# Optimization experiments

Hardware: AMD Instinct MI355X
Metric: run time of the kernel (lower is better)

Reference implementation:

```python
import math
import jax, jax.numpy as jnp
import numpy as np

DIM = 2048
N_HEADS = 16
HEAD_DIM = DIM // N_HEADS  # 128
BSZ = 2
SEQLEN = 2048
ROPE_THETA = 500000.0


def _make_freqs(seqlen, head_dim, theta):
    inv = 1.0 / (theta ** (np.arange(0, head_dim, 2, dtype=np.float32) / head_dim))
    t = np.arange(seqlen, dtype=np.float32)
    f = np.outer(t, inv)  # [S, hd//2]
    return jnp.asarray(np.cos(f)), jnp.asarray(np.sin(f))


def setup_inputs() -> dict:
    key = jax.random.key(0)
    kx, kq, kk, kv, ko = jax.random.split(key, 5)
    scale = 0.02
    x = jax.random.normal(kx, (BSZ, SEQLEN, DIM), dtype=jnp.float32)
    wq = jax.random.normal(kq, (DIM, DIM), dtype=jnp.float32) * scale
    wk = jax.random.normal(kk, (DIM, DIM), dtype=jnp.float32) * scale
    wv = jax.random.normal(kv, (DIM, DIM), dtype=jnp.float32) * scale
    wo = jax.random.normal(ko, (DIM, DIM), dtype=jnp.float32) * scale
    freqs_cos, freqs_sin = _make_freqs(SEQLEN, HEAD_DIM, ROPE_THETA)
    # causal additive mask: 0 on/below diag, -inf above
    mask = jnp.triu(jnp.full((SEQLEN, SEQLEN), float('-inf'), dtype=jnp.float32), k=1)
    return {"x": x, "start_pos": 0, "freqs_cos": freqs_cos, "freqs_sin": freqs_sin,
            "mask": mask, "wq": wq, "wk": wk, "wv": wv, "wo": wo}


def _apply_rope(t, cos, sin):
    # t: [B, S, H, hd]; cos/sin: [S, hd//2]
    b, s, h, hd = t.shape
    tr = t.reshape(b, s, h, hd // 2, 2)
    a, bb = tr[..., 0], tr[..., 1]
    c = cos[None, :, None, :]
    sn = sin[None, :, None, :]
    out_r = a * c - bb * sn
    out_i = a * sn + bb * c
    return jnp.stack([out_r, out_i], axis=-1).reshape(b, s, h, hd)


def reference(x, start_pos, freqs_cos, freqs_sin, mask, wq, wk, wv, wo):
    b, s, _ = x.shape
    xq = (x @ wq.T).reshape(b, s, N_HEADS, HEAD_DIM)
    xk = (x @ wk.T).reshape(b, s, N_HEADS, HEAD_DIM)
    xv = (x @ wv.T).reshape(b, s, N_HEADS, HEAD_DIM)
    xq = _apply_rope(xq, freqs_cos, freqs_sin)
    xk = _apply_rope(xk, freqs_cos, freqs_sin)
    # [B, H, S, hd]
    xq = xq.transpose(0, 2, 1, 3)
    xk = xk.transpose(0, 2, 1, 3)
    xv = xv.transpose(0, 2, 1, 3)
    scores = jnp.einsum('bhqd,bhkd->bhqk', xq, xk) / math.sqrt(HEAD_DIM)
    scores = scores + mask[None, None, :, :]
    probs = jax.nn.softmax(scores.astype(jnp.float32), axis=-1).astype(xq.dtype)
    out = jnp.einsum('bhqk,bhkd->bhqd', probs, xv)
    out = out.transpose(0, 2, 1, 3).reshape(b, s, -1)
    return out @ wo.T
```

## Files before the change

### kernel.cpp

```cpp
#include <hip/hip_runtime.h>
#include <stdint.h>

#define DIM 2048
#define SEQ 2048
#define NHEADS 16
#define HDIM 128
#define BSZ 2
#define ROWS (BSZ*SEQ)

typedef uint16_t u16;
typedef __attribute__((ext_vector_type(8))) short bf16x8;
typedef __attribute__((ext_vector_type(4))) short bf16x4;
typedef __attribute__((ext_vector_type(4))) float fx4;
typedef __attribute__((ext_vector_type(4))) uint16_t u16x4;

typedef const __attribute__((address_space(1))) uint32_t* gp_t;
typedef __attribute__((address_space(3))) uint32_t* lp_t;
#define GLL16(g, l) __builtin_amdgcn_global_load_lds((gp_t)(g), (lp_t)(l), 16, 0, 0)

__device__ inline u16 f2bf(float f) {
  union { float f; uint32_t u; } v; v.f = f;
  uint32_t u = v.u;
  u += 0x7FFFu + ((u >> 16) & 1u);
  return (u16)(u >> 16);
}
__device__ inline float bf2f(u16 h) {
  union { uint32_t u; float f; } v; v.u = ((uint32_t)h) << 16;
  return v.f;
}

__global__ __launch_bounds__(256) void cvt5_kernel(const float* __restrict__ sx,
    const float* __restrict__ s1, const float* __restrict__ s2,
    const float* __restrict__ s3, const float* __restrict__ s4,
    u16* __restrict__ dst) {
  const int XC = (ROWS * DIM) / 4;
  const int WC = (DIM * DIM) / 4;
  int i = blockIdx.x * 256 + threadIdx.x;
  const float* src;
  int off;
  if (i < XC) { src = sx; off = i; }
  else {
    int t = i - XC;
    int w = t >> 20;
    off = t & (WC - 1);
    src = (w == 0) ? s1 : (w == 1) ? s2 : (w == 2) ? s3 : s4;
  }
  fx4 f = *(const fx4*)(src + (size_t)off * 4);
  u16x4 o;
  o[0] = f2bf(f[0]); o[1] = f2bf(f[1]); o[2] = f2bf(f[2]); o[3] = f2bf(f[3]);
  *(u16x4*)(dst + (size_t)i * 4) = o;
}

__device__ inline void gemm128_core(const u16* __restrict__ A, const u16* __restrict__ B,
                                    u16 (&As)[128][32], u16 (&Bs)[128][32],
                                    fx4 (&acc)[4][4], int M0, int N0) {
  const int tid  = threadIdx.x;
  const int lane = tid & 63;
  const int wave = tid >> 6;
  const int wm = (wave >> 1) * 64;
  const int wn = (wave & 1) * 64;
  const int l16 = lane & 15;
  const int q8  = (lane >> 4) * 8;
#pragma unroll
  for (int tm = 0; tm < 4; ++tm)
#pragma unroll
    for (int tn = 0; tn < 4; ++tn) acc[tm][tn] = fx4{0.f, 0.f, 0.f, 0.f};

  const int wrow = wave * 32;
  const size_t laneA = (size_t)(M0 + wrow + (lane >> 2)) * DIM + (lane & 3) * 8;
  const size_t laneB = (size_t)(N0 + wrow + (lane >> 2)) * DIM + (lane & 3) * 8;

  for (int k0 = 0; k0 < DIM; k0 += 32) {
    __syncthreads();
    GLL16(A + laneA + k0,            &As[wrow][0]);
    GLL16(A + laneA + 16 * DIM + k0, &As[wrow + 16][0]);
    GLL16(B + laneB + k0,            &Bs[wrow][0]);
    GLL16(B + laneB + 16 * DIM + k0, &Bs[wrow + 16][0]);
    __syncthreads();
    bf16x8 af[4], bfr[4];
#pragma unroll
    for (int t = 0; t < 4; ++t) {
      af[t]  = *(const bf16x8*)&As[wm + t * 16 + l16][q8];
      bfr[t] = *(const bf16x8*)&Bs[wn + t * 16 + l16][q8];
    }
#pragma unroll
    for (int tm = 0; tm < 4; ++tm)
#pragma unroll
      for (int tn = 0; tn < 4; ++tn)
        acc[tm][tn] = __builtin_amdgcn_mfma_f32_16x16x32_bf16(af[tm], bfr[tn], acc[tm][tn], 0, 0, 0);
  }
}

#define BM 256
#define BN 128
#define BK 64
#define NT (DIM / BK)
#define BUFSZ ((BM + BN) * BK)

__global__ __launch_bounds__(512, 2) void gemm_qkv8(const u16* __restrict__ A,
    const u16* __restrict__ B0, const u16* __restrict__ B1, const u16* __restrict__ B2,
    u16* __restrict__ C0, u16* __restrict__ C1, u16* __restrict__ vtg,
    const float* __restrict__ fcos, const float* __restrict__ fsin) {
  __shared__ __align__(16) u16 sm[2 * BUFSZ];

  const int tid  = threadIdx.x;
  const int lane = tid & 63, wave = tid >> 6;
  const int l16  = lane & 15, quad = lane >> 4;
  const int wm   = wave >> 2;
  const int wn   = wave & 3;

  int t = (blockIdx.x & 7) * 96 + (blockIdx.x >> 3);
  const int z   = t >> 8;
  const int rem = t & 255;
  const int M0  = (rem >> 4) * BM;
  const int N0  = (rem & 15) * BN;
  const u16* B = (z == 0) ? B0 : (z == 1) ? B1 : B2;

  const int u0 = tid, u1 = 512 + tid;
  const int rl0 = u0 >> 3, ch0 = (u0 & 7) ^ (rl0 & 7);
  const int rl1 = u1 >> 3, ch1 = (u1 & 7) ^ (rl1 & 7);

  const int sw  = l16 & 7;
  const int ka0 = (quad ^ sw) * 8;
  const int ka1 = ((4 + quad) ^ sw) * 8;
  const int rowA = (wm * 128 + l16) * BK;
  const int rowB = (wn * 32  + l16) * BK;

#define STGA(h, kt2) do { if ((kt2) < NT) {                                              \
    const u16* _g = A + (size_t)(M0 + (h) * 128) * DIM + (kt2) * BK;                     \
    u16* _l = sm + ((kt2) & 1) * BUFSZ + (h) * 8192 + wave * 512;                        \
    GLL16(_g + (size_t)rl0 * DIM + ch0 * 8, _l);                                         \
    GLL16(_g + (size_t)rl1 * DIM + ch1 * 8, _l + 4096); } } while (0)
#define STGB(kt2) do { if ((kt2) < NT) {                                                 \
    const u16* _g = B + (size_t)N0 * DIM + (kt2) * BK;                                   \
    u16* _l = sm + ((kt2) & 1) * BUFSZ + 16384 + wave * 512;                             \
    GLL16(_g + (size_t)rl0 * DIM + ch0 * 8, _l);                                         \
    GLL16(_g + (size_t)rl1 * DIM + ch1 * 8, _l + 4096); } } while (0)

  STGB(0); STGA(0, 0); STGA(1, 0);
  STGB(1); STGA(0, 1);
  asm volatile("s_waitcnt vmcnt(4)" ::: "memory");
  __builtin_amdgcn_s_barrier();

  fx4 acc[8][2];
#pragma unroll
  for (int m = 0; m < 8; ++m)
#pragma unroll
    for (int n = 0; n < 2; ++n) acc[m][n] = fx4{0.f, 0.f, 0.f, 0.f};

  bf16x8 af[4][2], b0[2], b1[2];

  for (int kt = 0; kt < NT; ++kt) {
    const u16* Ab = sm + (kt & 1) * BUFSZ;
    const u16* Bb = Ab + 16384;

#pragma unroll
    for (int m = 0; m < 4; ++m) {
      af[m][0] = *(const bf16x8*)(Ab + rowA + m * (16 * BK) + ka0);
      af[m][1] = *(const bf16x8*)(Ab + rowA + m * (16 * BK) + ka1);
    }
    b0[0] = *(const bf16x8*)(Bb + rowB + ka0);
    b0[1] = *(const bf16x8*)(Bb + rowB + ka1);
    STGA(1, kt + 1);
    asm volatile("s_waitcnt lgkmcnt(8)" ::: "memory");
    __builtin_amdgcn_sched_barrier(0);
    __builtin_amdgcn_s_barrier();
    asm volatile("s_waitcnt lgkmcnt(0)" ::: "memory");
    __builtin_amdgcn_sched_barrier(0);
    __builtin_amdgcn_s_setprio(1);
#pragma unroll
    for (int m = 0; m < 4; ++m) {
      acc[m][0] = __builtin_amdgcn_mfma_f32_16x16x32_bf16(af[m][0], b0[0], acc[m][0], 0, 0, 0);
      acc[m][0] = __builtin_amdgcn_mfma_f32_16x16x32_bf16(af[m][1], b0[1], acc[m][0], 0, 0, 0);
    }
    __builtin_amdgcn_s_setprio(0);
    __builtin_amdgcn_s_barrier();

    b1[0] = *(const bf16x8*)(Bb + rowB + 16 * BK + ka0);
    b1[1] = *(const bf16x8*)(Bb + rowB + 16 * BK + ka1);
    __builtin_amdgcn_s_barrier();
    asm volatile("s_waitcnt lgkmcnt(0)" ::: "memory");
    __builtin_amdgcn_sched_barrier(0);
    __builtin_amdgcn_s_setprio(1);
#pragma unroll
    for (int m = 0; m < 4; ++m) {
      acc[m][1] = __builtin_amdgcn_mfma_f32_16x16x32_bf16(af[m][0], b1[0], acc[m][1], 0, 0, 0);
      acc[m][1] = __builtin_amdgcn_mfma_f32_16x16x32_bf16(af[m][1], b1[1], acc[m][1], 0, 0, 0);
    }
    __builtin_amdgcn_s_setprio(0);
    __builtin_amdgcn_s_barrier();

#pragma unroll
    for (int m = 0; m < 4; ++m) {
      af[m][0] = *(const bf16x8*)(Ab + rowA + (m + 4) * (16 * BK) + ka0);
      af[m][1] = *(const bf16x8*)(Ab + rowA + (m + 4) * (16 * BK) + ka1);
    }
    STGB(kt + 2);
    __builtin_amdgcn_s_barrier();
    asm volatile("s_waitcnt lgkmcnt(0)" ::: "memory");
    __builtin_amdgcn_sched_barrier(0);
    __builtin_amdgcn_s_setprio(1);
#pragma unroll
    for (int m = 0; m < 4; ++m) {
      acc[m + 4][1] = __builtin_amdgcn_mfma_f32_16x16x32_bf16(af[m][0], b1[0], acc[m + 4][1], 0, 0, 0);
      acc[m + 4][1] = __builtin_amdgcn_mfma_f32_16x16x32_bf16(af[m][1], b1[1], acc[m + 4][1], 0, 0, 0);
    }
    __builtin_amdgcn_s_setprio(0);
    __builtin_amdgcn_s_barrier();

    STGA(0, kt + 2);
    __builtin_amdgcn_s_barrier();
    __builtin_amdgcn_s_setprio(1);
#pragma unroll
    for (int m = 0; m < 4; ++m) {
      acc[m + 4][0] = __builtin_amdgcn_mfma_f32_16x16x32_bf16(af[m][0], b0[0], acc[m + 4][0], 0, 0, 0);
      acc[m + 4][0] = __builtin_amdgcn_mfma_f32_16x16x32_bf16(af[m][1], b0[1], acc[m + 4][0], 0, 0, 0);
    }
    __builtin_amdgcn_s_setprio(0);
    if (kt < NT - 2) asm volatile("s_waitcnt vmcnt(4)" ::: "memory");
    else             asm volatile("s_waitcnt vmcnt(0)" ::: "memory");
    __builtin_amdgcn_sched_barrier(0);
    __builtin_amdgcn_s_barrier();
  }
#undef STGA
#undef STGB

  if (z < 2) {
    u16* C = (z == 0) ? C0 : C1;
    u16* Cr = C + (size_t)(M0 + wm * 128 + quad * 4) * DIM + N0 + wn * 32 + l16;
#pragma unroll
    for (int mt = 0; mt < 8; ++mt)
#pragma unroll
      for (int r = 0; r < 4; ++r) {
        int s = (M0 + wm * 128 + mt * 16 + quad * 4 + r) & (SEQ - 1);
        const float* cb = fcos + s * 64;
        const float* sb = fsin + s * 64;
#pragma unroll
        for (int nt = 0; nt < 2; ++nt) {
          int p = (wn * 32 + nt * 16 + l16) >> 1;
          float val = acc[mt][nt][r];
          float par = __shfl_xor(val, 1);
          float c = cb[p], sn = sb[p];
          float out = (l16 & 1) ? (par * sn + val * c) : (val * c - par * sn);
          Cr[(size_t)(mt * 16 + r) * DIM + nt * 16] = f2bf(out);
        }
      }
  } else {
    u16 (*T)[256] = reinterpret_cast<u16 (*)[256]>(sm);
    __syncthreads();
#pragma unroll
    for (int mt = 0; mt < 8; ++mt)
#pragma unroll
      for (int nt = 0; nt < 2; ++nt) {
        int col = wn * 32 + nt * 16 + l16;
        int rowb = (wm * 128 + mt * 16 + quad * 4) ^ ((col & 7) << 3);
        u16x4 p;
        p[0] = f2bf(acc[mt][nt][0]); p[1] = f2bf(acc[mt][nt][1]);
        p[2] = f2bf(acc[mt][nt][2]); p[3] = f2bf(acc[mt][nt][3]);
        *(u16x4*)&T[col][rowb] = p;
      }
    __syncthreads();
    const int b  = M0 >> 11;
    const int s0 = M0 & (SEQ - 1);
    const int h  = N0 >> 7;
#pragma unroll
    for (int i = 0; i < 8; ++i) {
      int c = i * 512 + tid;
      int col = c >> 5;
      int s8 = (c & 31) * 8;
      bf16x8 v8 = *(const bf16x8*)&T[col][s8 ^ ((col & 7) << 3)];
      *(bf16x8*)(vtg + ((size_t)(b * NHEADS + h) * HDIM + col) * SEQ + s0 + s8) = v8;
    }
  }
}

__global__ __launch_bounds__(256) void gemm_out(const u16* __restrict__ A,
                                                const u16* __restrict__ B,
                                                float* __restrict__ C) {
  __shared__ __align__(16) u16 As[128][32];
  __shared__ __align__(16) u16 Bs[128][32];
  const int M0 = blockIdx.y * 128, N0 = blockIdx.x * 128;
  fx4 acc[4][4];
  gemm128_core(A, B, As, Bs, acc, M0, N0);
  const int lane = threadIdx.x & 63, wave = threadIdx.x >> 6;
  const int wm = (wave >> 1) * 64, wn = (wave & 1) * 64;
  const int l16 = lane & 15, quad = lane >> 4;
#pragma unroll
  for (int tm = 0; tm < 4; ++tm)
#pragma unroll
    for (int tn = 0; tn < 4; ++tn)
#pragma unroll
      for (int r = 0; r < 4; ++r) {
        size_t row = (size_t)(M0 + wm + tm * 16 + quad * 4 + r);
        size_t col = (size_t)(N0 + wn + tn * 16 + l16);
        C[row * DIM + col] = acc[tm][tn][r];
      }
}

struct SMemS { u16 Ks[64][136]; u16 Vt[128][72]; };
union SMemU { SMemS s; u16 Ot[4][32][136]; };

__global__ __launch_bounds__(256, 2) void attn_kernel(const u16* __restrict__ qm,
                                                      const u16* __restrict__ km,
                                                      const u16* __restrict__ vtg,
                                                      u16* __restrict__ ao) {
  __shared__ __align__(16) SMemU sm;
  const int tid = threadIdx.x;
  const int lane = tid & 63, wave = tid >> 6;
  const int l16 = lane & 15, quad = lane >> 4;
  const int idx = blockIdx.x;
  const int bh = idx & 31;
  const int j = idx >> 5;
  const int qt = (j < 8) ? (15 - j) : (j - 8);
  const int b = bh >> 4, h = bh & 15;
  const int q0 = qt * 128;
  const size_t brow = (size_t)b * SEQ;
  const int hc = h * HDIM;
  const size_t vbase = (size_t)bh * HDIM * SEQ;
  const int nkt = 2 * qt + 2;

  bf16x8 aq[2][4];
#pragma unroll
  for (int nt = 0; nt < 2; ++nt) {
    size_t qbase = (brow + q0 + wave * 32 + nt * 16 + l16) * DIM + hc;
#pragma unroll
    for (int dc = 0; dc < 4; ++dc)
      aq[nt][dc] = *(const bf16x8*)(qm + qbase + dc * 32 + quad * 8);
  }
  fx4 o[2][8];
#pragma unroll
  for (int nt = 0; nt < 2; ++nt)
#pragma unroll
    for (int dt = 0; dt < 8; ++dt) o[nt][dt] = fx4{0.f, 0.f, 0.f, 0.f};
  float mr[2] = {-3e38f, -3e38f}, lr[2] = {0.f, 0.f};

  bf16x8 kreg[4], vreg[4];
#pragma unroll
  for (int i = 0; i < 4; ++i) {
    int c = i * 256 + tid;
    kreg[i] = *(const bf16x8*)(km + (brow + (c >> 4)) * DIM + hc + (c & 15) * 8);
    vreg[i] = *(const bf16x8*)(vtg + vbase + (size_t)(c >> 3) * SEQ + (c & 7) * 8);
  }

  for (int kt = 0; kt < nkt; ++kt) {
    __syncthreads();
#pragma unroll
    for (int i = 0; i < 4; ++i) {
      int c = i * 256 + tid;
      *(bf16x8*)&sm.s.Ks[c >> 4][(c & 15) * 8] = kreg[i];
      *(bf16x8*)&sm.s.Vt[c >> 3][(c & 7) * 8] = vreg[i];
    }
    __syncthreads();
    if (kt + 1 < nkt) {
      const int kv1 = (kt + 1) * 64;
#pragma unroll
      for (int i = 0; i < 4; ++i) {
        int c = i * 256 + tid;
        kreg[i] = *(const bf16x8*)(km + (brow + kv1 + (c >> 4)) * DIM + hc + (c & 15) * 8);
        vreg[i] = *(const bf16x8*)(vtg + vbase + (size_t)(c >> 3) * SEQ + kv1 + (c & 7) * 8);
      }
    }
    fx4 s[2][4];
#pragma unroll
    for (int tm = 0; tm < 4; ++tm) {
      fx4 a0 = fx4{0.f, 0.f, 0.f, 0.f}, a1 = fx4{0.f, 0.f, 0.f, 0.f};
#pragma unroll
      for (int dc = 0; dc < 4; ++dc) {
        bf16x8 kf = *(const bf16x8*)&sm.s.Ks[tm * 16 + l16][dc * 32 + quad * 8];
        a0 = __builtin_amdgcn_mfma_f32_16x16x32_bf16(kf, aq[0][dc], a0, 0, 0, 0);
        a1 = __builtin_amdgcn_mfma_f32_16x16x32_bf16(kf, aq[1][dc], a1, 0, 0, 0);
      }
      s[0][tm] = a0 * 0.08838834764831845f;
      s[1][tm] = a1 * 0.08838834764831845f;
    }
    if (kt >= nkt - 2) {
      const int kv0 = kt * 64;
#pragma unroll
      for (int nt = 0; nt < 2; ++nt) {
        int qpos = q0 + wave * 32 + nt * 16 + l16;
#pragma unroll
        for (int tm = 0; tm < 4; ++tm)
#pragma unroll
          for (int r = 0; r < 4; ++r)
            if (kv0 + tm * 16 + quad * 4 + r > qpos) s[nt][tm][r] = -1e30f;
      }
    }
    float alpha[2];
    bf16x4 pf[2][4];
#pragma unroll
    for (int nt = 0; nt < 2; ++nt) {
      float t = -3e38f;
#pragma unroll
      for (int tm = 0; tm < 4; ++tm)
        t = fmaxf(t, fmaxf(fmaxf(s[nt][tm][0], s[nt][tm][1]),
                           fmaxf(s[nt][tm][2], s[nt][tm][3])));
      t = fmaxf(t, __shfl_xor(t, 16));
      t = fmaxf(t, __shfl_xor(t, 32));
      float mnew = fmaxf(mr[nt], t);
      alpha[nt] = __expf(mr[nt] - mnew);
      float sum = 0.f;
#pragma unroll
      for (int tm = 0; tm < 4; ++tm) {
        fx4 p;
#pragma unroll
        for (int r = 0; r < 4; ++r) {
          p[r] = __expf(s[nt][tm][r] - mnew);
          sum += p[r];
        }
        bf16x4 pb;
        pb[0] = (short)f2bf(p[0]); pb[1] = (short)f2bf(p[1]);
        pb[2] = (short)f2bf(p[2]); pb[3] = (short)f2bf(p[3]);
        pf[nt][tm] = pb;
      }
      sum += __shfl_xor(sum, 16);
      sum += __shfl_xor(sum, 32);
      lr[nt] = lr[nt] * alpha[nt] + sum;
      mr[nt] = mnew;
#pragma unroll
      for (int dt = 0; dt < 8; ++dt) o[nt][dt] *= alpha[nt];
    }
#pragma unroll
    for (int tm = 0; tm < 4; ++tm) {
#pragma unroll
      for (int dt = 0; dt < 8; ++dt) {
        bf16x4 vf = *(const bf16x4*)&sm.s.Vt[dt * 16 + l16][tm * 16 + quad * 4];
        o[0][dt] = __builtin_amdgcn_mfma_f32_16x16x16bf16_1k(vf, pf[0][tm], o[0][dt], 0, 0, 0);
        o[1][dt] = __builtin_amdgcn_mfma_f32_16x16x16bf16_1k(vf, pf[1][tm], o[1][dt], 0, 0, 0);
      }
    }
  }
  __syncthreads();
#pragma unroll
  for (int nt = 0; nt < 2; ++nt) {
    float inv = 1.f / lr[nt];
#pragma unroll
    for (int dt = 0; dt < 8; ++dt) {
      fx4 v = o[nt][dt];
      u16x4 p;
      p[0] = f2bf(v[0] * inv); p[1] = f2bf(v[1] * inv);
      p[2] = f2bf(v[2] * inv); p[3] = f2bf(v[3] * inv);
      *(u16x4*)&sm.Ot[wave][nt * 16 + l16][dt * 16 + quad * 4] = p;
    }
  }
#pragma unroll
  for (int i = 0; i < 8; ++i) {
    int c = i * 64 + lane;
    int row = c >> 4;
    int ch = c & 15;
    bf16x8 t = *(const bf16x8*)&sm.Ot[wave][row][ch * 8];
    *(bf16x8*)(ao + (brow + q0 + wave * 32 + row) * DIM + hc + ch * 8) = t;
  }
}

extern "C" void kernel_launch(void* const* d_in, const int* in_sizes, int n_in,
                              void* d_out, int out_size, void* d_ws, size_t ws_size,
                              hipStream_t stream) {
  const float* x    = (const float*)d_in[0];
  const float* fcos = (const float*)d_in[2];
  const float* fsin = (const float*)d_in[3];
  const float* wq   = (const float*)d_in[5];
  const float* wk   = (const float*)d_in[6];
  const float* wv   = (const float*)d_in[7];
  const float* wo   = (const float*)d_in[8];
  float* out = (float*)d_out;

  const size_t XN = (size_t)ROWS * DIM;
  const size_t WN = (size_t)DIM * DIM;
  u16* ws  = (u16*)d_ws;
  u16* xb  = ws;
  u16* wqb = xb + XN;
  u16* wkb = wqb + WN;
  u16* wvb = wkb + WN;
  u16* wob = wvb + WN;
  u16* q   = wob + WN;
  u16* k   = q + XN;
  u16* vtg = k + XN;
  u16* ao  = vtg + XN;

  const int total_chunks = (int)((XN + 4 * WN) / 4);
  cvt5_kernel<<<total_chunks / 256, 256, 0, stream>>>(x, wq, wk, wv, wo, ws);

  gemm_qkv8<<<dim3(768), 512, 0, stream>>>(xb, wqb, wkb, wvb, q, k, vtg, fcos, fsin);

  attn_kernel<<<dim3(512), 256, 0, stream>>>(q, k, vtg, ao);

  gemm_out<<<dim3(DIM / 128, ROWS / 128), 256, 0, stream>>>(ao, wob, out);
}
```

Baseline: 387.4 us.

## Replace output projection GEMM with 8-wave double-buffered 256x128 pipelined kernel

New measurement: 388.4 us. About the same (+0.2%).

```diff
diff --git a/kernel.cpp b/kernel.cpp
--- a/kernel.cpp
+++ b/kernel.cpp
@@ -51,46 +51,6 @@
   *(u16x4*)(dst + (size_t)i * 4) = o;
 }
 
-__device__ inline void gemm128_core(const u16* __restrict__ A, const u16* __restrict__ B,
-                                    u16 (&As)[128][32], u16 (&Bs)[128][32],
-                                    fx4 (&acc)[4][4], int M0, int N0) {
-  const int tid  = threadIdx.x;
-  const int lane = tid & 63;
-  const int wave = tid >> 6;
-  const int wm = (wave >> 1) * 64;
-  const int wn = (wave & 1) * 64;
-  const int l16 = lane & 15;
-  const int q8  = (lane >> 4) * 8;
-#pragma unroll
-  for (int tm = 0; tm < 4; ++tm)
-#pragma unroll
-    for (int tn = 0; tn < 4; ++tn) acc[tm][tn] = fx4{0.f, 0.f, 0.f, 0.f};
-
-  const int wrow = wave * 32;
-  const size_t laneA = (size_t)(M0 + wrow + (lane >> 2)) * DIM + (lane & 3) * 8;
-  const size_t laneB = (size_t)(N0 + wrow + (lane >> 2)) * DIM + (lane & 3) * 8;
-
-  for (int k0 = 0; k0 < DIM; k0 += 32) {
-    __syncthreads();
-    GLL16(A + laneA + k0,            &As[wrow][0]);
-    GLL16(A + laneA + 16 * DIM + k0, &As[wrow + 16][0]);
-    GLL16(B + laneB + k0,            &Bs[wrow][0]);
-    GLL16(B + laneB + 16 * DIM + k0, &Bs[wrow + 16][0]);
-    __syncthreads();
-    bf16x8 af[4], bfr[4];
-#pragma unroll
-    for (int t = 0; t < 4; ++t) {
-      af[t]  = *(const bf16x8*)&As[wm + t * 16 + l16][q8];
-      bfr[t] = *(const bf16x8*)&Bs[wn + t * 16 + l16][q8];
-    }
-#pragma unroll
-    for (int tm = 0; tm < 4; ++tm)
-#pragma unroll
-      for (int tn = 0; tn < 4; ++tn)
-        acc[tm][tn] = __builtin_amdgcn_mfma_f32_16x16x32_bf16(af[tm], bfr[tn], acc[tm][tn], 0, 0, 0);
-  }
-}
-
 #define BM 256
 #define BN 128
 #define BK 64
@@ -274,27 +234,138 @@
   }
 }
 
-__global__ __launch_bounds__(256) void gemm_out(const u16* __restrict__ A,
-                                                const u16* __restrict__ B,
-                                                float* __restrict__ C) {
-  __shared__ __align__(16) u16 As[128][32];
-  __shared__ __align__(16) u16 Bs[128][32];
-  const int M0 = blockIdx.y * 128, N0 = blockIdx.x * 128;
-  fx4 acc[4][4];
-  gemm128_core(A, B, As, Bs, acc, M0, N0);
-  const int lane = threadIdx.x & 63, wave = threadIdx.x >> 6;
-  const int wm = (wave >> 1) * 64, wn = (wave & 1) * 64;
-  const int l16 = lane & 15, quad = lane >> 4;
-#pragma unroll
-  for (int tm = 0; tm < 4; ++tm)
-#pragma unroll
-    for (int tn = 0; tn < 4; ++tn)
-#pragma unroll
-      for (int r = 0; r < 4; ++r) {
-        size_t row = (size_t)(M0 + wm + tm * 16 + quad * 4 + r);
-        size_t col = (size_t)(N0 + wn + tn * 16 + l16);
-        C[row * DIM + col] = acc[tm][tn][r];
-      }
+__global__ __launch_bounds__(512, 2) void gemm_out8(const u16* __restrict__ A,
+                                                    const u16* __restrict__ B,
+                                                    float* __restrict__ C) {
+  __shared__ __align__(16) u16 sm[2 * BUFSZ];
+
+  const int tid  = threadIdx.x;
+  const int lane = tid & 63, wave = tid >> 6;
+  const int l16  = lane & 15, quad = lane >> 4;
+  const int wm   = wave >> 2;
+  const int wn   = wave & 3;
+
+  int t = (blockIdx.x & 7) * 32 + (blockIdx.x >> 3);
+  const int M0  = (t >> 4) * BM;
+  const int N0  = (t & 15) * BN;
+
+  const int u0 = tid, u1 = 512 + tid;
+  const int rl0 = u0 >> 3, ch0 = (u0 & 7) ^ (rl0 & 7);
+  const int rl1 = u1 >> 3, ch1 = (u1 & 7) ^ (rl1 & 7);
+
+  const int sw  = l16 & 7;
+  const int ka0 = (quad ^ sw) * 8;
+  const int ka1 = ((4 + quad) ^ sw) * 8;
+  const int rowA = (wm * 128 + l16) * BK;
+  const int rowB = (wn * 32  + l16) * BK;
+
+#define STGA(h, kt2) do { if ((kt2) < NT) {                                              \
+    const u16* _g = A + (size_t)(M0 + (h) * 128) * DIM + (kt2) * BK;                     \
+    u16* _l = sm + ((kt2) & 1) * BUFSZ + (h) * 8192 + wave * 512;                        \
+    GLL16(_g + (size_t)rl0 * DIM + ch0 * 8, _l);                                         \
+    GLL16(_g + (size_t)rl1 * DIM + ch1 * 8, _l + 4096); } } while (0)
+#define STGB(kt2) do { if ((kt2) < NT) {                                                 \
+    const u16* _g = B + (size_t)N0 * DIM + (kt2) * BK;                                   \
+    u16* _l = sm + ((kt2) & 1) * BUFSZ + 16384 + wave * 512;                             \
+    GLL16(_g + (size_t)rl0 * DIM + ch0 * 8, _l);                                         \
+    GLL16(_g + (size_t)rl1 * DIM + ch1 * 8, _l + 4096); } } while (0)
+
+  STGB(0); STGA(0, 0); STGA(1, 0);
+  STGB(1); STGA(0, 1);
+  asm volatile("s_waitcnt vmcnt(4)" ::: "memory");
+  __builtin_amdgcn_s_barrier();
+
+  fx4 acc[8][2];
+#pragma unroll
+  for (int m = 0; m < 8; ++m)
+#pragma unroll
+    for (int n = 0; n < 2; ++n) acc[m][n] = fx4{0.f, 0.f, 0.f, 0.f};
+
+  bf16x8 af[4][2], b0[2], b1[2];
+
+  for (int kt = 0; kt < NT; ++kt) {
+    const u16* Ab = sm + (kt & 1) * BUFSZ;
+    const u16* Bb = Ab + 16384;
+
+#pragma unroll
+    for (int m = 0; m < 4; ++m) {
+      af[m][0] = *(const bf16x8*)(Ab + rowA + m * (16 * BK) + ka0);
+      af[m][1] = *(const bf16x8*)(Ab + rowA + m * (16 * BK) + ka1);
+    }
+    b0[0] = *(const bf16x8*)(Bb + rowB + ka0);
+    b0[1] = *(const bf16x8*)(Bb + rowB + ka1);
+    STGA(1, kt + 1);
+    asm volatile("s_waitcnt lgkmcnt(8)" ::: "memory");
+    __builtin_amdgcn_sched_barrier(0);
+    __builtin_amdgcn_s_barrier();
+    asm volatile("s_waitcnt lgkmcnt(0)" ::: "memory");
+    __builtin_amdgcn_sched_barrier(0);
+    __builtin_amdgcn_s_setprio(1);
+#pragma unroll
+    for (int m = 0; m < 4; ++m) {
+      acc[m][0] = __builtin_amdgcn_mfma_f32_16x16x32_bf16(af[m][0], b0[0], acc[m][0], 0, 0, 0);
+      acc[m][0] = __builtin_amdgcn_mfma_f32_16x16x32_bf16(af[m][1], b0[1], acc[m][0], 0, 0, 0);
+    }
+    __builtin_amdgcn_s_setprio(0);
+    __builtin_amdgcn_s_barrier();
+
+    b1[0] = *(const bf16x8*)(Bb + rowB + 16 * BK + ka0);
+    b1[1] = *(const bf16x8*)(Bb + rowB + 16 * BK + ka1);
+    __builtin_amdgcn_s_barrier();
+    asm volatile("s_waitcnt lgkmcnt(0)" ::: "memory");
+    __builtin_amdgcn_sched_barrier(0);
+    __builtin_amdgcn_s_setprio(1);
+#pragma unroll
+    for (int m = 0; m < 4; ++m) {
+      acc[m][1] = __builtin_amdgcn_mfma_f32_16x16x32_bf16(af[m][0], b1[0], acc[m][1], 0, 0, 0);
+      acc[m][1] = __builtin_amdgcn_mfma_f32_16x16x32_bf16(af[m][1], b1[1], acc[m][1], 0, 0, 0);
+    }
+    __builtin_amdgcn_s_setprio(0);
+    __builtin_amdgcn_s_barrier();
+
+#pragma unroll
+    for (int m = 0; m < 4; ++m) {
+      af[m][0] = *(const bf16x8*)(Ab + rowA + (m + 4) * (16 * BK) + ka0);
+      af[m][1] = *(const bf16x8*)(Ab + rowA + (m + 4) * (16 * BK) + ka1);
+    }
+    STGB(kt + 2);
+    __builtin_amdgcn_s_barrier();
+    asm volatile("s_waitcnt lgkmcnt(0)" ::: "memory");
+    __builtin_amdgcn_sched_barrier(0);
+    __builtin_amdgcn_s_setprio(1);
+#pragma unroll
+    for (int m = 0; m < 4; ++m) {
+      acc[m + 4][1] = __builtin_amdgcn_mfma_f32_16x16x32_bf16(af[m][0], b1[0], acc[m + 4][1], 0, 0, 0);
+      acc[m + 4][1] = __builtin_amdgcn_mfma_f32_16x16x32_bf16(af[m][1], b1[1], acc[m + 4][1], 0, 0, 0);
+    }
+    __builtin_amdgcn_s_setprio(0);
+    __builtin_amdgcn_s_barrier();
+
+    STGA(0, kt + 2);
+    __builtin_amdgcn_s_barrier();
+    __builtin_amdgcn_s_setprio(1);
+#pragma unroll
+    for (int m = 0; m < 4; ++m) {
+      acc[m + 4][0] = __builtin_amdgcn_mfma_f32_16x16x32_bf16(af[m][0], b0[0], acc[m + 4][0], 0, 0, 0);
+      acc[m + 4][0] = __builtin_amdgcn_mfma_f32_16x16x32_bf16(af[m][1], b0[1], acc[m + 4][0], 0, 0, 0);
+    }
+    __builtin_amdgcn_s_setprio(0);
+    if (kt < NT - 2) asm volatile("s_waitcnt vmcnt(4)" ::: "memory");
+    else             asm volatile("s_waitcnt vmcnt(0)" ::: "memory");
+    __builtin_amdgcn_sched_barrier(0);
+    __builtin_amdgcn_s_barrier();
+  }
+#undef STGA
+#undef STGB
+
+  float* Cr = C + (size_t)(M0 + wm * 128 + quad * 4) * DIM + N0 + wn * 32 + l16;
+#pragma unroll
+  for (int mt = 0; mt < 8; ++mt)
+#pragma unroll
+    for (int nt = 0; nt < 2; ++nt)
+#pragma unroll
+      for (int r = 0; r < 4; ++r)
+        Cr[(size_t)(mt * 16 + r) * DIM + nt * 16] = acc[mt][nt][r];
 }
 
 struct SMemS { u16 Ks[64][136]; u16 Vt[128][72]; };
@@ -484,5 +555,5 @@
 
   attn_kernel<<<dim3(512), 256, 0, stream>>>(q, k, vtg, ao);
 
-  gemm_out<<<dim3(DIM / 128, ROWS / 128), 256, 0, stream>>>(ao, wob, out);
-}
+  gemm_out8<<<dim3(256), 512, 0, stream>>>(ao, wob, out);
+}
```
